# Kernel optimization log

Measured on AMD Instinct MI355X. Metric: run time of the kernel, lower is better.

The kernel has to match this reference:

```python
import jax, jax.numpy as jnp
import numpy as np

N = 100000
E = 1600000
D_IN = 128
F = 128


def _glorot(key, shape, scale=1.0):
    fan_in, fan_out = shape
    std = jnp.sqrt(2.0 / (fan_in + fan_out))
    return jax.random.normal(key, shape, dtype=jnp.float32) * std * scale


def setup_inputs() -> dict:
    key = jax.random.key(0)
    ks = jax.random.split(key, 10)
    h = jax.random.normal(ks[0], (N, D_IN), dtype=jnp.float32)
    # ensure every node appears as a row (src) so degree >= 1 (no inf in deg**-0.5)
    src_extra = jax.random.randint(ks[1], (E - N,), 0, N, dtype=jnp.int32)
    edge_src = jnp.concatenate([jnp.arange(N, dtype=jnp.int32), src_extra])
    edge_dst = jax.random.randint(ks[2], (E,), 0, N, dtype=jnp.int32)
    # faithful to original: fake indices sampled in [0, E) (jnp indexing clamps)
    src_fake = jax.random.randint(ks[3], (E,), 0, E, dtype=jnp.int32)
    dst_fake = jax.random.randint(ks[4], (E,), 0, E, dtype=jnp.int32)
    w_gcn0 = _glorot(ks[5], (D_IN, F))
    w_gcn1 = _glorot(ks[6], (F, F))
    # small scale on rate0 head to keep exp(sum over F dims) finite in fp32
    w_rate0 = _glorot(ks[7], (F, F), scale=0.05)
    w_rate1 = _glorot(ks[8], (F, 1))
    w_alpha = _glorot(ks[9], (F, 1))
    return {"h": h, "w_gcn0": w_gcn0, "w_gcn1": w_gcn1, "w_rate0": w_rate0,
            "w_rate1": w_rate1, "w_alpha": w_alpha, "edge_src": edge_src,
            "edge_dst": edge_dst, "src_fake": src_fake, "dst_fake": dst_fake}


def _gcn(h, W, norm, edge_src, edge_dst):
    h = h * norm                     # [N, d] degree pre-norm
    h = h @ W                        # dense projection
    h = jax.ops.segment_sum(h[edge_dst], edge_src, num_segments=N)  # a @ h
    return h * norm                  # degree post-norm


def reference(h, w_gcn0, w_gcn1, w_rate0, w_rate1, w_alpha,
              edge_src, edge_dst, src_fake, dst_fake):
    ones = jnp.ones((E,), dtype=h.dtype)
    deg = jax.ops.segment_sum(ones, edge_src, num_segments=N)  # row sums of a
    norm = (deg ** -0.5)[:, None]

    h = _gcn(h, w_gcn0, norm, edge_src, edge_dst)
    h = _gcn(h, w_gcn1, norm, edge_src, edge_dst)

    rate0 = h @ w_rate0   # [N, F]
    rate1 = h @ w_rate1   # [N, 1]
    alpha = h @ w_alpha   # [N, 1]

    src, dst = edge_src, edge_dst
    rate0_real = jnp.exp((rate0[src] + rate0[dst]).sum(-1))
    rate1_real = jnp.exp((rate1[src] + rate1[dst]).sum(-1))
    alpha_real = jax.nn.sigmoid((alpha[src] * alpha[dst]).sum(-1) / alpha.shape[-1] ** 0.5)

    # faithful to original (including rate0+rate1 mix and /shape (not sqrt) in alpha_fake)
    rate0_fake = jnp.exp((rate0[src_fake] + rate1[dst_fake]).sum(-1))
    rate1_fake = jnp.exp((rate1[src_fake] + rate1[dst_fake]).sum(-1))
    alpha_fake = jax.nn.sigmoid((alpha[src] * alpha[dst_fake]).sum(-1) / alpha.shape[-1])

    return jnp.stack([rate0_real, rate1_real, alpha_real,
                      rate0_fake, rate1_fake, alpha_fake])  # [6, E]
```

## Files before the change

kernel.cpp:

```cpp
#include <hip/hip_runtime.h>
#include <hip/hip_bf16.h>
#include <math.h>

#define NN 100000
#define EE 1600000
#define KB 256
#define RR 391
#define CAP 8192


__global__ __launch_bounds__(256) void k_partA(const int* __restrict__ src, const int* __restrict__ dst,
                                               int* __restrict__ gcur, unsigned int* __restrict__ pk, int E,
                                               const float* __restrict__ w_gcn0, const float* __restrict__ w_gcn1,
                                               const float* __restrict__ w_rate0, const float* __restrict__ w_rate1,
                                               const float* __restrict__ w_alpha, float* __restrict__ P) {
    __shared__ int cnt[KB];
    __shared__ int base[KB];
    int t = threadIdx.x;
    int e0 = blockIdx.x * 4096;
    int rem = E - e0;
    cnt[t] = 0;
    __syncthreads();
    unsigned int pkv[16];
    int bkt[16];
    int rnk[16];
    const int4* src4 = (const int4*)(src + e0);
    const int4* dst4 = (const int4*)(dst + e0);
    #pragma unroll
    for (int j = 0; j < 4; ++j) {
        int o = t * 16 + j * 4;
        if (o < rem) {
            int4 s4 = src4[t * 4 + j];
            int4 d4 = dst4[t * 4 + j];
            int ss[4] = {s4.x, s4.y, s4.z, s4.w};
            int dd[4] = {d4.x, d4.y, d4.z, d4.w};
            #pragma unroll
            for (int k = 0; k < 4; ++k) {
                int b = ss[k] / RR;
                int idx = j * 4 + k;
                bkt[idx] = b;
                pkv[idx] = (unsigned int)dd[k] | ((unsigned int)(ss[k] - b * RR) << 17);
                rnk[idx] = atomicAdd(&cnt[b], 1);
            }
        } else {
            #pragma unroll
            for (int k = 0; k < 4; ++k) bkt[j * 4 + k] = -1;
        }
    }
    __syncthreads();
    base[t] = (cnt[t] > 0) ? atomicAdd(&gcur[t], cnt[t]) : 0;
    __syncthreads();
    #pragma unroll
    for (int i = 0; i < 16; ++i) {
        if (bkt[i] >= 0) {
            int rel = base[bkt[i]] + rnk[i];
            if (rel < CAP) pk[bkt[i] * CAP + rel] = pkv[i];
        }
    }
    if (blockIdx.x == 0) {
        __shared__ float V0[128], V1[128], V2[128];
        __shared__ float Q0[128], Q1[128], Q2[128];
        if (t < 128) {
            float s = 0.f;
            for (int j = 0; j < 128; ++j) s += w_rate0[t * 128 + j];
            V0[t] = s; V1[t] = w_rate1[t]; V2[t] = w_alpha[t];
        }
        __syncthreads();
        if (t < 128) {
            float q0 = 0.f, q1 = 0.f, q2 = 0.f;
            for (int k = 0; k < 128; ++k) {
                float w = w_gcn1[t * 128 + k];
                q0 += w * V0[k]; q1 += w * V1[k]; q2 += w * V2[k];
            }
            Q0[t] = q0; Q1[t] = q1; Q2[t] = q2;
        }
        __syncthreads();
        if (t < 128) {
            float p0 = 0.f, p1 = 0.f, p2 = 0.f;
            for (int m = 0; m < 128; ++m) {
                float w = w_gcn0[t * 128 + m];
                p0 += w * Q0[m]; p1 += w * Q1[m]; p2 += w * Q2[m];
            }
            P[t] = p0; P[128 + t] = p1; P[256 + t] = p2;
        }
    }
}


__global__ __launch_bounds__(1024) void k_cnt_proj(const unsigned int* __restrict__ pk,
                                                   const int* __restrict__ gcur,
                                                   const float* __restrict__ h,
                                                   const float* __restrict__ P,
                                                   float* __restrict__ nrm, float4* __restrict__ w4, int n) {
    __shared__ int c[RR];
    __shared__ float s_nrm[RR];
    __shared__ float sP[384];
    int b = blockIdx.x;
    int t = threadIdx.x;
    int nlo = b * RR;
    int nhi = nlo + RR; if (nhi > n) nhi = n;
    if (nlo >= n) return;
    int nn = nhi - nlo;
    if (t < 384) sP[t] = P[t];
    for (int i = t; i < RR; i += 1024) c[i] = 0;
    __syncthreads();
    int P0 = b * CAP;
    int m = gcur[b]; if (m > CAP) m = CAP;
    for (int i = t; i < m; i += 1024) atomicAdd(&c[pk[P0 + i] >> 17], 1);
    __syncthreads();
    for (int i = t; i < nn; i += 1024) {
        float nv = rsqrtf((float)c[i]);
        s_nrm[i] = nv;
        nrm[nlo + i] = nv;
    }
    __syncthreads();
    int hw = t >> 5;
    int l32 = t & 31;
    int c4 = l32 * 4;
    float4 c0 = *(const float4*)(sP + c4);
    float4 c1 = *(const float4*)(sP + 128 + c4);
    float4 c2 = *(const float4*)(sP + 256 + c4);
    for (int i0 = 0; i0 < nn; i0 += 32) {
        int i = i0 + hw;
        if (i >= nn) break;
        int node = nlo + i;
        float4 hv = *(const float4*)(h + (size_t)node * 128 + c4);
        float p0 = hv.x * c0.x + hv.y * c0.y + hv.z * c0.z + hv.w * c0.w;
        float p1 = hv.x * c1.x + hv.y * c1.y + hv.z * c1.z + hv.w * c1.w;
        float p2 = hv.x * c2.x + hv.y * c2.y + hv.z * c2.z + hv.w * c2.w;
        #pragma unroll
        for (int off = 16; off > 0; off >>= 1) {
            p0 += __shfl_down(p0, off, 32);
            p1 += __shfl_down(p1, off, 32);
            p2 += __shfl_down(p2, off, 32);
        }
        if (l32 == 0) {
            float nv = s_nrm[i];
            w4[node] = make_float4(nv * p0, nv * p1, nv * p2, 0.f);
        }
    }
}


__global__ __launch_bounds__(1024) void k_agg(const unsigned int* __restrict__ pk,
                                              const int* __restrict__ gcur,
                                              const float4* __restrict__ T, const float* __restrict__ nrm,
                                              float4* __restrict__ outv, int n, int mode) {
    __shared__ float s0[RR], s1[RR], s2[RR];
    int b = blockIdx.x;
    int t = threadIdx.x;
    int nlo = b * RR;
    int nhi = nlo + RR; if (nhi > n) nhi = n;
    if (nlo >= n) return;
    for (int i = t; i < RR; i += 1024) { s0[i] = 0.f; s1[i] = 0.f; s2[i] = 0.f; }
    __syncthreads();
    int P0 = b * CAP;
    int m = gcur[b]; if (m > CAP) m = CAP;
    unsigned int w[8];
    float4 v[8];
    bool ok[8];
    #pragma unroll
    for (int j = 0; j < 8; ++j) {
        int i = t + j * 1024;
        ok[j] = i < m;
        if (ok[j]) w[j] = pk[P0 + i];
    }
    #pragma unroll
    for (int j = 0; j < 8; ++j) {
        if (ok[j]) v[j] = T[w[j] & 0x1FFFFu];
    }
    #pragma unroll
    for (int j = 0; j < 8; ++j) {
        if (ok[j]) {
            int srel = (int)(w[j] >> 17);
            atomicAdd(&s0[srel], v[j].x);
            atomicAdd(&s1[srel], v[j].y);
            atomicAdd(&s2[srel], v[j].z);
        }
    }
    __syncthreads();
    int nn = nhi - nlo;
    for (int i = t; i < nn; i += 1024) {
        int node = nlo + i;
        float nv = nrm[node];
        float sc = (mode == 1) ? nv * nv : nv;
        outv[node] = make_float4(sc * s0[i], sc * s1[i], sc * s2[i], 0.f);
    }
}


__global__ __launch_bounds__(256) void k_edge_out(const int* __restrict__ esrc, const int* __restrict__ edst,
                                                  const int* __restrict__ sfake, const int* __restrict__ dfake,
                                                  const float4* __restrict__ p4, float* __restrict__ out,
                                                  int E, int n) {
    int e = (blockIdx.x * 256 + threadIdx.x) * 4;
    if (e >= E) return;
    int4 s4 = *(const int4*)(esrc + e);
    int4 d4 = *(const int4*)(edst + e);
    int4 sf4 = *(const int4*)(sfake + e);
    int4 df4 = *(const int4*)(dfake + e);
    int ss[4] = {s4.x, s4.y, s4.z, s4.w};
    int dd[4] = {d4.x, d4.y, d4.z, d4.w};
    int sf[4] = {sf4.x, sf4.y, sf4.z, sf4.w};
    int df[4] = {df4.x, df4.y, df4.z, df4.w};
    float4 o0, o1, o2, o3, o4o, o5;
    float* po0 = (float*)&o0; float* po1 = (float*)&o1; float* po2 = (float*)&o2;
    float* po3 = (float*)&o3; float* po4 = (float*)&o4o; float* po5 = (float*)&o5;
    #pragma unroll
    for (int k = 0; k < 4; ++k) {
        int sfc = sf[k] < 0 ? 0 : (sf[k] >= n ? n - 1 : sf[k]);
        int dfc = df[k] < 0 ? 0 : (df[k] >= n ? n - 1 : df[k]);
        float4 ps = p4[ss[k]], pd = p4[dd[k]], psf = p4[sfc], pdf = p4[dfc];
        po0[k] = expf(ps.x + pd.x);
        po1[k] = expf(ps.y + pd.y);
        po2[k] = 1.f / (1.f + expf(-(ps.z * pd.z)));
        po3[k] = expf(psf.x + 128.f * pdf.y);
        po4[k] = expf(psf.y + pdf.y);
        po5[k] = 1.f / (1.f + expf(-(ps.z * pdf.z)));
    }
    *(float4*)(out + e)                 = o0;
    *(float4*)(out + (size_t)E + e)     = o1;
    *(float4*)(out + (size_t)2 * E + e) = o2;
    *(float4*)(out + (size_t)3 * E + e) = o3;
    *(float4*)(out + (size_t)4 * E + e) = o4o;
    *(float4*)(out + (size_t)5 * E + e) = o5;
}


extern "C" void kernel_launch(void* const* d_in, const int* in_sizes, int n_in,
                              void* d_out, int out_size, void* d_ws, size_t ws_size,
                              hipStream_t stream) {
    const float* h       = (const float*)d_in[0];
    const float* w_gcn0  = (const float*)d_in[1];
    const float* w_gcn1  = (const float*)d_in[2];
    const float* w_rate0 = (const float*)d_in[3];
    const float* w_rate1 = (const float*)d_in[4];
    const float* w_alpha = (const float*)d_in[5];
    const int* edge_src  = (const int*)d_in[6];
    const int* edge_dst  = (const int*)d_in[7];
    const int* src_fake  = (const int*)d_in[8];
    const int* dst_fake  = (const int*)d_in[9];
    float* out = (float*)d_out;

    const int N = NN, E = EE;

    char* p = (char*)d_ws;
    auto alloc = [&](size_t bytes) {
        char* r = p;
        p += (bytes + 255) & ~(size_t)255;
        return r;
    };
    unsigned int* pk = (unsigned int*)alloc((size_t)KB * CAP * 4);
    int* gcur   = (int*)alloc(KB * 4);
    float* nrm  = (float*)alloc((size_t)N * 4);
    float4* w4  = (float4*)alloc((size_t)N * 16);
    float4* z4  = (float4*)alloc((size_t)N * 16);
    float4* p4  = (float4*)alloc((size_t)N * 16);
    float* P    = (float*)alloc(384 * 4);

    hipMemsetAsync(gcur, 0, KB * 4, stream);

    int ebl4k = (E + 4095) / 4096;

    k_partA<<<ebl4k, 256, 0, stream>>>(edge_src, edge_dst, gcur, pk, E,
                                       w_gcn0, w_gcn1, w_rate0, w_rate1, w_alpha, P);
    k_cnt_proj<<<KB, 1024, 0, stream>>>(pk, gcur, h, P, nrm, w4, N);
    k_agg<<<KB, 1024, 0, stream>>>(pk, gcur, w4, nrm, z4, N, 1);
    k_agg<<<KB, 1024, 0, stream>>>(pk, gcur, z4, nrm, p4, N, 2);
    k_edge_out<<<(E / 4 + 255) / 256, 256, 0, stream>>>(edge_src, edge_dst, src_fake, dst_fake, p4, out, E, N);
}
```

Before: 249.4 us.

## Fuse projection, two aggregations and edge output into one cooperative kernel

Replaces four kernel launches (count/projection, two aggregations, edge output) with a single cooperative kernel that separates the phases with grid-wide syncs. The per-block degree norms stay in shared memory across phases instead of being written to and re-read from a global buffer. The aggregation loops also drop the 8-way register-batched gather in favour of a simple strided loop. The edge-output phase now runs on only 256 blocks of 1024 threads, which may reduce latency hiding for its random gathers, and each grid sync has its own cost.

```diff
diff --git a/kernel.cpp b/kernel.cpp
--- a/kernel.cpp
+++ b/kernel.cpp
@@ -1,6 +1,9 @@
 #include <hip/hip_runtime.h>
+#include <hip/hip_cooperative_groups.h>
 #include <hip/hip_bf16.h>
 #include <math.h>
+
+namespace cg = cooperative_groups;
 
 #define NN 100000
 #define EE 1600000
@@ -87,143 +90,128 @@
 }
 
 
-__global__ __launch_bounds__(1024) void k_cnt_proj(const unsigned int* __restrict__ pk,
-                                                   const int* __restrict__ gcur,
-                                                   const float* __restrict__ h,
-                                                   const float* __restrict__ P,
-                                                   float* __restrict__ nrm, float4* __restrict__ w4, int n) {
-    __shared__ int c[RR];
-    __shared__ float s_nrm[RR];
+__global__ __launch_bounds__(1024) void k_rest(const unsigned int* __restrict__ pk,
+                                               const int* __restrict__ gcur,
+                                               const float* __restrict__ h,
+                                               const float* __restrict__ P,
+                                               const int* __restrict__ esrc, const int* __restrict__ edst,
+                                               const int* __restrict__ sfake, const int* __restrict__ dfake,
+                                               float4* __restrict__ w4, float4* __restrict__ z4,
+                                               float4* __restrict__ p4, float* __restrict__ out) {
+    cg::grid_group grid = cg::this_grid();
+    const int b = blockIdx.x;
+    const int t = threadIdx.x;
+
+    __shared__ int   ci[RR];
+    __shared__ float sn[RR];
+    __shared__ float s0[RR], s1[RR], s2[RR];
     __shared__ float sP[384];
-    int b = blockIdx.x;
-    int t = threadIdx.x;
-    int nlo = b * RR;
-    int nhi = nlo + RR; if (nhi > n) nhi = n;
-    if (nlo >= n) return;
-    int nn = nhi - nlo;
+
+    const int nlo = b * RR;
+    int nhi = nlo + RR; if (nhi > NN) nhi = NN;
+    const int nn = nhi - nlo;
+    const int P0 = b * CAP;
+    int m = gcur[b]; if (m > CAP) m = CAP;
+
     if (t < 384) sP[t] = P[t];
-    for (int i = t; i < RR; i += 1024) c[i] = 0;
-    __syncthreads();
-    int P0 = b * CAP;
-    int m = gcur[b]; if (m > CAP) m = CAP;
-    for (int i = t; i < m; i += 1024) atomicAdd(&c[pk[P0 + i] >> 17], 1);
+    for (int i = t; i < RR; i += 1024) ci[i] = 0;
+    __syncthreads();
+    for (int i = t; i < m; i += 1024) atomicAdd(&ci[pk[P0 + i] >> 17], 1);
+    __syncthreads();
+    for (int i = t; i < nn; i += 1024) sn[i] = rsqrtf((float)ci[i]);
+    __syncthreads();
+    {
+        int hw = t >> 5, l32 = t & 31, c4 = l32 * 4;
+        float4 c0 = *(const float4*)(sP + c4);
+        float4 c1 = *(const float4*)(sP + 128 + c4);
+        float4 c2 = *(const float4*)(sP + 256 + c4);
+        for (int i = hw; i < nn; i += 32) {
+            int node = nlo + i;
+            float4 hv = *(const float4*)(h + (size_t)node * 128 + c4);
+            float p0 = hv.x * c0.x + hv.y * c0.y + hv.z * c0.z + hv.w * c0.w;
+            float p1 = hv.x * c1.x + hv.y * c1.y + hv.z * c1.z + hv.w * c1.w;
+            float p2 = hv.x * c2.x + hv.y * c2.y + hv.z * c2.z + hv.w * c2.w;
+            #pragma unroll
+            for (int off = 16; off > 0; off >>= 1) {
+                p0 += __shfl_down(p0, off, 32);
+                p1 += __shfl_down(p1, off, 32);
+                p2 += __shfl_down(p2, off, 32);
+            }
+            if (l32 == 0) {
+                float nv = sn[i];
+                w4[node] = make_float4(nv * p0, nv * p1, nv * p2, 0.f);
+            }
+        }
+    }
+    grid.sync();
+
+    for (int i = t; i < RR; i += 1024) { s0[i] = 0.f; s1[i] = 0.f; s2[i] = 0.f; }
+    __syncthreads();
+    for (int i = t; i < m; i += 1024) {
+        unsigned int w = pk[P0 + i];
+        int srel = (int)(w >> 17);
+        float4 v = w4[w & 0x1FFFFu];
+        atomicAdd(&s0[srel], v.x);
+        atomicAdd(&s1[srel], v.y);
+        atomicAdd(&s2[srel], v.z);
+    }
     __syncthreads();
     for (int i = t; i < nn; i += 1024) {
-        float nv = rsqrtf((float)c[i]);
-        s_nrm[i] = nv;
-        nrm[nlo + i] = nv;
-    }
-    __syncthreads();
-    int hw = t >> 5;
-    int l32 = t & 31;
-    int c4 = l32 * 4;
-    float4 c0 = *(const float4*)(sP + c4);
-    float4 c1 = *(const float4*)(sP + 128 + c4);
-    float4 c2 = *(const float4*)(sP + 256 + c4);
-    for (int i0 = 0; i0 < nn; i0 += 32) {
-        int i = i0 + hw;
-        if (i >= nn) break;
-        int node = nlo + i;
-        float4 hv = *(const float4*)(h + (size_t)node * 128 + c4);
-        float p0 = hv.x * c0.x + hv.y * c0.y + hv.z * c0.z + hv.w * c0.w;
-        float p1 = hv.x * c1.x + hv.y * c1.y + hv.z * c1.z + hv.w * c1.w;
-        float p2 = hv.x * c2.x + hv.y * c2.y + hv.z * c2.z + hv.w * c2.w;
+        float nv = sn[i];
+        float sc = nv * nv;
+        z4[nlo + i] = make_float4(sc * s0[i], sc * s1[i], sc * s2[i], 0.f);
+    }
+    grid.sync();
+
+    __syncthreads();
+    for (int i = t; i < RR; i += 1024) { s0[i] = 0.f; s1[i] = 0.f; s2[i] = 0.f; }
+    __syncthreads();
+    for (int i = t; i < m; i += 1024) {
+        unsigned int w = pk[P0 + i];
+        int srel = (int)(w >> 17);
+        float4 v = z4[w & 0x1FFFFu];
+        atomicAdd(&s0[srel], v.x);
+        atomicAdd(&s1[srel], v.y);
+        atomicAdd(&s2[srel], v.z);
+    }
+    __syncthreads();
+    for (int i = t; i < nn; i += 1024) {
+        float nv = sn[i];
+        p4[nlo + i] = make_float4(nv * s0[i], nv * s1[i], nv * s2[i], 0.f);
+    }
+    grid.sync();
+
+    for (int e = (b * 1024 + t) * 4; e < EE; e += KB * 1024 * 4) {
+        int4 s4 = *(const int4*)(esrc + e);
+        int4 d4 = *(const int4*)(edst + e);
+        int4 sf4 = *(const int4*)(sfake + e);
+        int4 df4 = *(const int4*)(dfake + e);
+        int ss[4] = {s4.x, s4.y, s4.z, s4.w};
+        int dd[4] = {d4.x, d4.y, d4.z, d4.w};
+        int sf[4] = {sf4.x, sf4.y, sf4.z, sf4.w};
+        int df[4] = {df4.x, df4.y, df4.z, df4.w};
+        float4 o0, o1, o2, o3, o4o, o5;
+        float* po0 = (float*)&o0; float* po1 = (float*)&o1; float* po2 = (float*)&o2;
+        float* po3 = (float*)&o3; float* po4 = (float*)&o4o; float* po5 = (float*)&o5;
         #pragma unroll
-        for (int off = 16; off > 0; off >>= 1) {
-            p0 += __shfl_down(p0, off, 32);
-            p1 += __shfl_down(p1, off, 32);
-            p2 += __shfl_down(p2, off, 32);
-        }
-        if (l32 == 0) {
-            float nv = s_nrm[i];
-            w4[node] = make_float4(nv * p0, nv * p1, nv * p2, 0.f);
-        }
-    }
-}
-
-
-__global__ __launch_bounds__(1024) void k_agg(const unsigned int* __restrict__ pk,
-                                              const int* __restrict__ gcur,
-                                              const float4* __restrict__ T, const float* __restrict__ nrm,
-                                              float4* __restrict__ outv, int n, int mode) {
-    __shared__ float s0[RR], s1[RR], s2[RR];
-    int b = blockIdx.x;
-    int t = threadIdx.x;
-    int nlo = b * RR;
-    int nhi = nlo + RR; if (nhi > n) nhi = n;
-    if (nlo >= n) return;
-    for (int i = t; i < RR; i += 1024) { s0[i] = 0.f; s1[i] = 0.f; s2[i] = 0.f; }
-    __syncthreads();
-    int P0 = b * CAP;
-    int m = gcur[b]; if (m > CAP) m = CAP;
-    unsigned int w[8];
-    float4 v[8];
-    bool ok[8];
-    #pragma unroll
-    for (int j = 0; j < 8; ++j) {
-        int i = t + j * 1024;
-        ok[j] = i < m;
-        if (ok[j]) w[j] = pk[P0 + i];
-    }
-    #pragma unroll
-    for (int j = 0; j < 8; ++j) {
-        if (ok[j]) v[j] = T[w[j] & 0x1FFFFu];
-    }
-    #pragma unroll
-    for (int j = 0; j < 8; ++j) {
-        if (ok[j]) {
-            int srel = (int)(w[j] >> 17);
-            atomicAdd(&s0[srel], v[j].x);
-            atomicAdd(&s1[srel], v[j].y);
-            atomicAdd(&s2[srel], v[j].z);
-        }
-    }
-    __syncthreads();
-    int nn = nhi - nlo;
-    for (int i = t; i < nn; i += 1024) {
-        int node = nlo + i;
-        float nv = nrm[node];
-        float sc = (mode == 1) ? nv * nv : nv;
-        outv[node] = make_float4(sc * s0[i], sc * s1[i], sc * s2[i], 0.f);
-    }
-}
-
-
-__global__ __launch_bounds__(256) void k_edge_out(const int* __restrict__ esrc, const int* __restrict__ edst,
-                                                  const int* __restrict__ sfake, const int* __restrict__ dfake,
-                                                  const float4* __restrict__ p4, float* __restrict__ out,
-                                                  int E, int n) {
-    int e = (blockIdx.x * 256 + threadIdx.x) * 4;
-    if (e >= E) return;
-    int4 s4 = *(const int4*)(esrc + e);
-    int4 d4 = *(const int4*)(edst + e);
-    int4 sf4 = *(const int4*)(sfake + e);
-    int4 df4 = *(const int4*)(dfake + e);
-    int ss[4] = {s4.x, s4.y, s4.z, s4.w};
-    int dd[4] = {d4.x, d4.y, d4.z, d4.w};
-    int sf[4] = {sf4.x, sf4.y, sf4.z, sf4.w};
-    int df[4] = {df4.x, df4.y, df4.z, df4.w};
-    float4 o0, o1, o2, o3, o4o, o5;
-    float* po0 = (float*)&o0; float* po1 = (float*)&o1; float* po2 = (float*)&o2;
-    float* po3 = (float*)&o3; float* po4 = (float*)&o4o; float* po5 = (float*)&o5;
-    #pragma unroll
-    for (int k = 0; k < 4; ++k) {
-        int sfc = sf[k] < 0 ? 0 : (sf[k] >= n ? n - 1 : sf[k]);
-        int dfc = df[k] < 0 ? 0 : (df[k] >= n ? n - 1 : df[k]);
-        float4 ps = p4[ss[k]], pd = p4[dd[k]], psf = p4[sfc], pdf = p4[dfc];
-        po0[k] = expf(ps.x + pd.x);
-        po1[k] = expf(ps.y + pd.y);
-        po2[k] = 1.f / (1.f + expf(-(ps.z * pd.z)));
-        po3[k] = expf(psf.x + 128.f * pdf.y);
-        po4[k] = expf(psf.y + pdf.y);
-        po5[k] = 1.f / (1.f + expf(-(ps.z * pdf.z)));
-    }
-    *(float4*)(out + e)                 = o0;
-    *(float4*)(out + (size_t)E + e)     = o1;
-    *(float4*)(out + (size_t)2 * E + e) = o2;
-    *(float4*)(out + (size_t)3 * E + e) = o3;
-    *(float4*)(out + (size_t)4 * E + e) = o4o;
-    *(float4*)(out + (size_t)5 * E + e) = o5;
+        for (int k = 0; k < 4; ++k) {
+            int sfc = sf[k] < 0 ? 0 : (sf[k] >= NN ? NN - 1 : sf[k]);
+            int dfc = df[k] < 0 ? 0 : (df[k] >= NN ? NN - 1 : df[k]);
+            float4 ps = p4[ss[k]], pd = p4[dd[k]], psf = p4[sfc], pdf = p4[dfc];
+            po0[k] = expf(ps.x + pd.x);
+            po1[k] = expf(ps.y + pd.y);
+            po2[k] = 1.f / (1.f + expf(-(ps.z * pd.z)));
+            po3[k] = expf(psf.x + 128.f * pdf.y);
+            po4[k] = expf(psf.y + pdf.y);
+            po5[k] = 1.f / (1.f + expf(-(ps.z * pdf.z)));
+        }
+        *(float4*)(out + e)                  = o0;
+        *(float4*)(out + (size_t)EE + e)     = o1;
+        *(float4*)(out + (size_t)2 * EE + e) = o2;
+        *(float4*)(out + (size_t)3 * EE + e) = o3;
+        *(float4*)(out + (size_t)4 * EE + e) = o4o;
+        *(float4*)(out + (size_t)5 * EE + e) = o5;
+    }
 }
 
 
@@ -242,7 +230,7 @@
     const int* dst_fake  = (const int*)d_in[9];
     float* out = (float*)d_out;
 
-    const int N = NN, E = EE;
+    const int E = EE;
 
     char* p = (char*)d_ws;
     auto alloc = [&](size_t bytes) {
@@ -252,20 +240,19 @@
     };
     unsigned int* pk = (unsigned int*)alloc((size_t)KB * CAP * 4);
     int* gcur   = (int*)alloc(KB * 4);
-    float* nrm  = (float*)alloc((size_t)N * 4);
-    float4* w4  = (float4*)alloc((size_t)N * 16);
-    float4* z4  = (float4*)alloc((size_t)N * 16);
-    float4* p4  = (float4*)alloc((size_t)N * 16);
+    float4* w4  = (float4*)alloc((size_t)NN * 16);
+    float4* z4  = (float4*)alloc((size_t)NN * 16);
+    float4* p4  = (float4*)alloc((size_t)NN * 16);
     float* P    = (float*)alloc(384 * 4);
 
     hipMemsetAsync(gcur, 0, KB * 4, stream);
 
     int ebl4k = (E + 4095) / 4096;
-
     k_partA<<<ebl4k, 256, 0, stream>>>(edge_src, edge_dst, gcur, pk, E,
                                        w_gcn0, w_gcn1, w_rate0, w_rate1, w_alpha, P);
-    k_cnt_proj<<<KB, 1024, 0, stream>>>(pk, gcur, h, P, nrm, w4, N);
-    k_agg<<<KB, 1024, 0, stream>>>(pk, gcur, w4, nrm, z4, N, 1);
-    k_agg<<<KB, 1024, 0, stream>>>(pk, gcur, z4, nrm, p4, N, 2);
-    k_edge_out<<<(E / 4 + 255) / 256, 256, 0, stream>>>(edge_src, edge_dst, src_fake, dst_fake, p4, out, E, N);
+
+    void* args[] = { (void*)&pk, (void*)&gcur, (void*)&h, (void*)&P,
+                     (void*)&edge_src, (void*)&edge_dst, (void*)&src_fake, (void*)&dst_fake,
+                     (void*)&w4, (void*)&z4, (void*)&p4, (void*)&out };
+    hipLaunchCooperativeKernel((void*)k_rest, dim3(KB), dim3(1024), args, 0, stream);
 }
```

New measurement: 345.1 us. +38.4%, slower.
